# Kernel optimization log

Hardware: AMD Instinct MI355X
Metric: run time of the kernel (lower is better)

## Reference

```python
import jax
import jax.numpy as jnp
from jax import lax
import numpy as np

B, H, W, C = 8, 128, 128, 64
KH, KW = 3, 3
K = KH * KW
OUT = 64
PAD = 1  # 'same' padding for 3x3, stride 1, dilation 1


def setup_inputs() -> dict:
    key = jax.random.key(0)
    k1, k2, k3, k4 = jax.random.split(key, 4)
    scale = 0.05  # keep learned offsets in a sane pixel range
    x = jax.random.normal(k1, (B, H, W, C), dtype=jnp.float32)
    offset_kernel = jax.random.normal(k2, (KH, KW, C, 2 * K), dtype=jnp.float32) * scale
    mask_kernel = jax.random.normal(k3, (KH, KW, C, K), dtype=jnp.float32) * scale
    filt = jax.random.normal(k4, (OUT, C, KH, KW), dtype=jnp.float32) * scale
    return {"x": x, "offset_kernel": offset_kernel, "mask_kernel": mask_kernel, "filt": filt}


def _conv_same(x, kernel):
    # x: [B,H,W,C], kernel: [kh,kw,Cin,Cout] -> [B,H,W,Cout]
    return lax.conv_general_dilated(
        x, kernel, window_strides=(1, 1), padding='SAME',
        dimension_numbers=('NHWC', 'HWIO', 'NHWC'))


def _bilinear_gather(img, py, px):
    # img: [B,C,H,W]; py,px: [B,K,H,W] float sampling coords (zero outside image)
    b, c, h, w = img.shape
    imf = img.reshape(b, c, h * w)
    y0 = jnp.floor(py)
    x0 = jnp.floor(px)
    ly = py - y0
    lx = px - x0

    def corner(yi, xi, wgt):
        valid = (yi >= 0) & (yi <= h - 1) & (xi >= 0) & (xi <= w - 1)
        yc = jnp.clip(yi, 0, h - 1).astype(jnp.int32)
        xc = jnp.clip(xi, 0, w - 1).astype(jnp.int32)
        idx = yc * w + xc  # [B,K,H,W]
        v = jax.vmap(lambda im, ix: jnp.take(im, ix, axis=1))(imf, idx)  # [B,C,K,H,W]
        return v * (wgt * valid.astype(img.dtype))[:, None]

    return (corner(y0, x0, (1 - ly) * (1 - lx))
            + corner(y0, x0 + 1, (1 - ly) * lx)
            + corner(y0 + 1, x0, ly * (1 - lx))
            + corner(y0 + 1, x0 + 1, ly * lx))


def reference(x, offset_kernel, mask_kernel, filt):
    # offset conv and mask conv (mask goes through sigmoid), both channels_last
    offset = _conv_same(x, offset_kernel)                 # [B,H,W,2K]
    mask = jax.nn.sigmoid(_conv_same(x, mask_kernel))     # [B,H,W,K]

    xc = jnp.transpose(x, (0, 3, 1, 2))                   # [B,C,H,W]
    off = jnp.transpose(offset, (0, 3, 1, 2)).reshape(B, K, 2, H, W)
    dy, dx = off[:, :, 0], off[:, :, 1]                   # [B,K,H,W]
    m = jnp.transpose(mask, (0, 3, 1, 2))                 # [B,K,H,W]

    # base sampling grid: p = out_loc + kernel_offset - pad + learned offset
    hh = jnp.arange(H, dtype=jnp.float32)
    ww = jnp.arange(W, dtype=jnp.float32)
    ky = jnp.repeat(jnp.arange(KH, dtype=jnp.float32), KW)  # [K]
    kx = jnp.tile(jnp.arange(KW, dtype=jnp.float32), KH)    # [K]
    py = hh[None, None, :, None] + (ky - PAD)[None, :, None, None] + dy  # [B,K,H,W]
    px = ww[None, None, None, :] + (kx - PAD)[None, :, None, None] + dx

    cols = _bilinear_gather(xc, py, px)                   # [B,C,K,H,W]
    cols = cols * m[:, None]                              # modulated (offset_groups=1)

    fk = filt.reshape(OUT, C, K)
    out = jnp.einsum('bcknm,ock->bonm', cols, fk)         # [B,OUT,H,W]
    return jnp.transpose(out, (0, 2, 3, 1))               # NHWC, bias disabled
```

## Files before the change

### kernel.cpp

```cpp
#include <hip/hip_runtime.h>
#include <math.h>

#define BB 8
#define HH 128
#define WW 128
#define CC 64
#define KK 9
#define OUTC 64
#define TW 16
#define KTOT 576
#define NELEM (BB*HH*WW*CC)
#define XSW 3456

typedef __attribute__((ext_vector_type(8))) short short8v;
typedef __attribute__((ext_vector_type(4))) float float4v;

static __device__ __forceinline__ unsigned short f2bf(float f) {
    unsigned int u = __float_as_uint(f);
    return (unsigned short)((u + 0x7FFFu + ((u >> 16) & 1u)) >> 16);
}
static __device__ __forceinline__ float bf2f(unsigned short h) {
    return __uint_as_float(((unsigned int)h) << 16);
}
static __device__ __forceinline__ float bf2f_lo(unsigned int w) {
    return __uint_as_float(w << 16);
}
static __device__ __forceinline__ float bf2f_hi(unsigned int w) {
    return __uint_as_float(w & 0xFFFF0000u);
}

static __device__ __forceinline__ int frag_addr(int p, int kappa) {
    int chunk = kappa >> 3;
    return ((chunk >> 2) << 9) + ((chunk & 3) << 7) + ((p ^ (chunk & 7)) << 3) + (kappa & 7);
}

__global__ __launch_bounds__(256) void prep_all(
    const float* __restrict__ x, const float* __restrict__ offk,
    const float* __restrict__ mk, const float* __restrict__ filt,
    unsigned short* __restrict__ fbf,
    unsigned short* __restrict__ wcf,
    unsigned short* __restrict__ xh,
    unsigned short* __restrict__ xl,
    int do_x)
{
    int bid = blockIdx.x, tid = threadIdx.x;
    if (bid < 144) {
        int j = bid * 256 + tid;
        {
            int w = j / 9216, rem = j - w * 9216;
            int ks = rem >> 9, ln = (rem >> 3) & 63, sj = rem & 7;
            int pl = ln & 15, lg = ln >> 4;
            int o = w * 16 + pl, kap = ks * 32 + lg * 8 + sj;
            int k = kap >> 6, c = kap & 63;
            fbf[j] = f2bf(filt[(o * CC + c) * KK + k]);
        }
        if (j < 18432) {
            int nh = j / 9216, rem = j - nh * 9216;
            int ks = rem >> 9, ln = (rem >> 3) & 63, sj = rem & 7;
            int pl = ln & 15, lg = ln >> 4;
            int o = nh * 16 + pl, kap = ks * 32 + lg * 8 + sj;
            int k = kap >> 6, c = kap & 63;
            float v = 0.f;
            if (o < 18)      v = offk[(k * CC + c) * 18 + o];
            else if (o < 27) v = mk[(k * CC + c) * 9 + (o - 18)];
            wcf[j] = f2bf(v);
        }
        return;
    }
    if (!do_x) return;
    int i = (bid - 144) * 256 + tid;
    const float* src = x + (size_t)i * 8;
    float4 a = *(const float4*)(src);
    float4 c = *(const float4*)(src + 4);
    float v[8] = {a.x, a.y, a.z, a.w, c.x, c.y, c.z, c.w};
    unsigned hq[4], lq[4];
#pragma unroll
    for (int j = 0; j < 4; ++j) {
        unsigned short h0 = f2bf(v[2 * j]),     h1 = f2bf(v[2 * j + 1]);
        unsigned short l0 = f2bf(v[2 * j] - bf2f(h0));
        unsigned short l1 = f2bf(v[2 * j + 1] - bf2f(h1));
        hq[j] = (unsigned)h0 | ((unsigned)h1 << 16);
        lq[j] = (unsigned)l0 | ((unsigned)l1 << 16);
    }
    *(uint4*)(xh + (size_t)i * 8) = make_uint4(hq[0], hq[1], hq[2], hq[3]);
    *(uint4*)(xl + (size_t)i * 8) = make_uint4(lq[0], lq[1], lq[2], lq[3]);
}

template<int HASB>
__global__ __launch_bounds__(256, 7) void deform_conv_fused(
    const float* __restrict__ x,
    const unsigned short* __restrict__ xh,
    const unsigned short* __restrict__ xl,
    const unsigned short* __restrict__ fbf,
    const unsigned short* __restrict__ wcf,
    float* __restrict__ out)
{
    __shared__ __align__(16) unsigned short ims[TW * KTOT];
    __shared__ __align__(16) union UU {
        float ps2[4][TW][18];
        struct { int4 c[144]; float4 w[144]; } gs;
    } u;

    const int tid  = threadIdx.x;
    const int lane = tid & 63;
    const int wave = tid >> 6;
    const int pl = lane & 15;
    const int lg = lane >> 4;
    const int off_e = lg * 128 + ((pl ^ lg) << 3);
    const int off_o = lg * 128 + ((pl ^ (lg + 4)) << 3);

    const int swz = (blockIdx.x & 7) * 1024 + (blockIdx.x >> 3);
    const int bw = swz & 7;
    const int h  = (swz >> 3) & 127;
    const int b  = swz >> 10;
    const int w0 = bw * TW;

    for (int e = tid; e < 864; e += 256) {
        int pln  = e / 432;
        int rem  = e - pln * 432;
        int r    = rem / 144;
        int rem2 = rem - r * 144;
        int px   = rem2 >> 3;
        int c8   = rem2 & 7;
        int y = h + r - 1, xg = w0 + px - 1;
        int lidx = (r * 18 + px) * 64 + ((c8 * 8) ^ ((px & 7) << 3)) + pln * XSW;
        uint4 val = make_uint4(0u, 0u, 0u, 0u);
        if ((unsigned)y < (unsigned)HH && (unsigned)xg < (unsigned)WW) {
            int goff = ((b * HH + y) * WW + xg) * CC + c8 * 8;
            if (HASB) {
                val = *(const uint4*)((pln ? xl : xh) + goff);
            } else {
                float4 v0 = *(const float4*)(x + goff);
                float4 v1 = *(const float4*)(x + goff + 4);
                float vv[8] = {v0.x, v0.y, v0.z, v0.w, v1.x, v1.y, v1.z, v1.w};
                unsigned short q[8];
#pragma unroll
                for (int j = 0; j < 8; ++j) {
                    unsigned short h0 = f2bf(vv[j]);
                    q[j] = pln ? f2bf(vv[j] - bf2f(h0)) : h0;
                }
                val = make_uint4((unsigned)q[0] | ((unsigned)q[1] << 16),
                                 (unsigned)q[2] | ((unsigned)q[3] << 16),
                                 (unsigned)q[4] | ((unsigned)q[5] << 16),
                                 (unsigned)q[6] | ((unsigned)q[7] << 16));
            }
        }
        *(uint4*)(ims + lidx) = val;
    }
    __syncthreads();

    const int nh = wave & 1, kh = wave >> 1;
    float4v acch = {0.f, 0.f, 0.f, 0.f}, accl = {0.f, 0.f, 0.f, 0.f};
    __builtin_amdgcn_s_setprio(1);
#pragma unroll
    for (int ks9 = 0; ks9 < 9; ++ks9) {
        const int ksg = kh * 9 + ks9;
        const int tap = ksg >> 1;
        const int cb  = (ksg & 1) * 32 + lg * 8;
        const int ky = tap / 3, kx = tap - ky * 3;
        const int px = pl + kx;
        const int base = (ky * 18 + px) * 64 + (cb ^ ((px & 7) << 3));
        short8v ahf = *(const short8v*)(ims + base);
        short8v alf = *(const short8v*)(ims + XSW + base);
        short8v bv  = *(const short8v*)(wcf + ((nh * 18 + ksg) << 9) + (lane << 3));
        acch = __builtin_amdgcn_mfma_f32_16x16x32_bf16(ahf, bv, acch, 0, 0, 0);
        accl = __builtin_amdgcn_mfma_f32_16x16x32_bf16(alf, bv, accl, 0, 0, 0);
    }
    __builtin_amdgcn_s_setprio(0);
#pragma unroll
    for (int r = 0; r < 4; ++r)
        u.ps2[wave][lg * 4 + r][pl] = acch[r] + accl[r];

    const unsigned short* Bpf = fbf + ((wave * 18) << 9) + (lane << 3);
    short8v bp0 = *(const short8v*)(Bpf);
    short8v bp1 = *(const short8v*)(Bpf + 512);
    __syncthreads();

    const int sp = tid / 9, sk = tid - (tid / 9) * 9;
    float s_dy = 0.f, s_dx = 0.f, s_ml = 0.f;
    if (tid < 144) {
        auto rd = [&](int o) {
            int nhh = o >> 4, col = o & 15;
            return u.ps2[nhh][sp][col] + u.ps2[2 + nhh][sp][col];
        };
        s_dy = rd(2 * sk); s_dx = rd(2 * sk + 1); s_ml = rd(18 + sk);
    }
    __syncthreads();

    if (tid < 144) {
        float m  = 1.f / (1.f + __expf(-s_ml));
        float py = (float)(h + (sk / 3) - 1) + s_dy;
        float px = (float)(w0 + sp + (sk % 3) - 1) + s_dx;
        float y0 = floorf(py), x0 = floorf(px);
        float ly = py - y0, lx = px - x0;
        bool vy0 = (y0 >= 0.f)  && (y0 <= 127.f);
        bool vy1 = (y0 >= -1.f) && (y0 <= 126.f);
        bool vx0 = (x0 >= 0.f)  && (x0 <= 127.f);
        bool vx1 = (x0 >= -1.f) && (x0 <= 126.f);
        float wy0 = 1.f - ly, wx0 = 1.f - lx;
        int iy0 = (int)fminf(fmaxf(y0, 0.f), 127.f);
        int iy1 = (int)fminf(fmaxf(y0 + 1.f, 0.f), 127.f);
        int ix0 = (int)fminf(fmaxf(x0, 0.f), 127.f);
        int ix1 = (int)fminf(fmaxf(x0 + 1.f, 0.f), 127.f);
        int base = b * (HH * WW * CC);
        u.gs.c[tid] = make_int4(base + (iy0 * WW + ix0) * CC,
                                base + (iy0 * WW + ix1) * CC,
                                base + (iy1 * WW + ix0) * CC,
                                base + (iy1 * WW + ix1) * CC);
        u.gs.w[tid] = make_float4((vy0 && vx0) ? wy0 * wx0 * m : 0.f,
                                  (vy0 && vx1) ? wy0 * lx  * m : 0.f,
                                  (vy1 && vx0) ? ly  * wx0 * m : 0.f,
                                  (vy1 && vx1) ? ly  * lx  * m : 0.f);
    }
    __syncthreads();

    if (HASB) {
        for (int t = tid; t < 1152; t += 256) {
            int pair = t >> 3, c8 = t & 7;
            int p = pair / 9, k = pair - (pair / 9) * 9;
            int4   cc = u.gs.c[pair];
            float4 wv = u.gs.w[pair];
            int co = c8 * 8;
            uint4 u00 = *(const uint4*)(xh + cc.x + co);
            uint4 u01 = *(const uint4*)(xh + cc.y + co);
            uint4 u10 = *(const uint4*)(xh + cc.z + co);
            uint4 u11 = *(const uint4*)(xh + cc.w + co);
            const unsigned* a00 = (const unsigned*)&u00;
            const unsigned* a01 = (const unsigned*)&u01;
            const unsigned* a10 = (const unsigned*)&u10;
            const unsigned* a11 = (const unsigned*)&u11;
            unsigned qq[4];
#pragma unroll
            for (int jj = 0; jj < 4; ++jj) {
                float rl = wv.x * bf2f_lo(a00[jj]) + wv.y * bf2f_lo(a01[jj])
                         + wv.z * bf2f_lo(a10[jj]) + wv.w * bf2f_lo(a11[jj]);
                float rh = wv.x * bf2f_hi(a00[jj]) + wv.y * bf2f_hi(a01[jj])
                         + wv.z * bf2f_hi(a10[jj]) + wv.w * bf2f_hi(a11[jj]);
                qq[jj] = (unsigned)f2bf(rl) | ((unsigned)f2bf(rh) << 16);
            }
            *(uint4*)(ims + frag_addr(p, k * 64 + co)) = make_uint4(qq[0], qq[1], qq[2], qq[3]);
        }
    } else {
        for (int t = tid; t < 1152; t += 256) {
            int pair = t >> 3, c8 = t & 7;
            int p = pair / 9, k = pair - (pair / 9) * 9;
            int4   cc = u.gs.c[pair];
            float4 wv = u.gs.w[pair];
            int co = c8 * 8;
            float r[8];
#pragma unroll
            for (int half = 0; half < 2; ++half) {
                float4 v00 = *(const float4*)(x + cc.x + co + half * 4);
                float4 v01 = *(const float4*)(x + cc.y + co + half * 4);
                float4 v10 = *(const float4*)(x + cc.z + co + half * 4);
                float4 v11 = *(const float4*)(x + cc.w + co + half * 4);
                r[half * 4 + 0] = wv.x * v00.x + wv.y * v01.x + wv.z * v10.x + wv.w * v11.x;
                r[half * 4 + 1] = wv.x * v00.y + wv.y * v01.y + wv.z * v10.y + wv.w * v11.y;
                r[half * 4 + 2] = wv.x * v00.z + wv.y * v01.z + wv.z * v10.z + wv.w * v11.z;
                r[half * 4 + 3] = wv.x * v00.w + wv.y * v01.w + wv.z * v10.w + wv.w * v11.w;
            }
            unsigned qq[4];
#pragma unroll
            for (int jj = 0; jj < 4; ++jj)
                qq[jj] = (unsigned)f2bf(r[2 * jj]) | ((unsigned)f2bf(r[2 * jj + 1]) << 16);
            *(uint4*)(ims + frag_addr(p, k * 64 + co)) = make_uint4(qq[0], qq[1], qq[2], qq[3]);
        }
    }
    __syncthreads();

    {
        float4v accA = {0.f, 0.f, 0.f, 0.f}, accB = {0.f, 0.f, 0.f, 0.f};
        __builtin_amdgcn_s_setprio(1);
#pragma unroll
        for (int ks = 0; ks < 18; ++ks) {
            short8v a  = *(const short8v*)(ims + ks * 512 + ((ks & 1) ? off_o : off_e));
            short8v bv = (ks == 0) ? bp0 : (ks == 1) ? bp1
                       : *(const short8v*)(Bpf + (ks << 9));
            if (ks & 1) accB = __builtin_amdgcn_mfma_f32_16x16x32_bf16(a, bv, accB, 0, 0, 0);
            else        accA = __builtin_amdgcn_mfma_f32_16x16x32_bf16(a, bv, accA, 0, 0, 0);
        }
        __builtin_amdgcn_s_setprio(0);
        const int o = wave * 16 + pl;
        const size_t rowbase = (size_t)(b * HH + h) * WW + w0;
#pragma unroll
        for (int r = 0; r < 4; ++r) {
            int p = lg * 4 + r;
            out[(rowbase + p) * OUTC + o] = accA[r] + accB[r];
        }
    }
}

extern "C" void kernel_launch(void* const* d_in, const int* in_sizes, int n_in,
                              void* d_out, int out_size, void* d_ws, size_t ws_size,
                              hipStream_t stream) {
    const float* x    = (const float*)d_in[0];
    const float* offk = (const float*)d_in[1];
    const float* mk   = (const float*)d_in[2];
    const float* filt = (const float*)d_in[3];
    float* out = (float*)d_out;
    unsigned short* fbf = (unsigned short*)d_ws;
    unsigned short* wcf = fbf + OUTC * KTOT;
    unsigned short* xh  = wcf + 32 * KTOT;
    unsigned short* xl  = xh + NELEM;
    size_t need = (size_t)(OUTC + 32) * KTOT * 2 + (size_t)NELEM * 4;
    int do_x = (ws_size >= need) ? 1 : 0;
    prep_all<<<144 + (do_x ? 4096 : 0), 256, 0, stream>>>(x, offk, mk, filt, fbf, wcf, xh, xl, do_x);
    if (do_x)
        deform_conv_fused<1><<<BB * HH * (WW / TW), 256, 0, stream>>>(x, xh, xl, fbf, wcf, out);
    else
        deform_conv_fused<0><<<BB * HH * (WW / TW), 256, 0, stream>>>(x, xh, xl, fbf, wcf, out);
}
```

Before: 80.09 us.

## Switch from split-bf16 to single fp16 storage and fp16 MFMA

Replaces the hi/lo bf16 split of x with one fp16 copy, so the offset/mask conv needs one MFMA stream instead of two, and prep writes half the data. The main MFMA now runs in f16 with the same instruction shape. Bilinear sampling weights are stored as packed half2 and the interpolation uses __hfma2 packed-half arithmetic. This cuts prep-time memory traffic, LDS staging and gather bandwidth. The cost is precision: fp16 has less range than bf16, and accumulating the interpolation in half may change the results.

```diff
diff --git a/kernel.cpp b/kernel.cpp
--- a/kernel.cpp
+++ b/kernel.cpp
@@ -1,4 +1,5 @@
 #include <hip/hip_runtime.h>
+#include <hip/hip_fp16.h>
 #include <math.h>
 
 #define BB 8
@@ -12,21 +13,18 @@
 #define NELEM (BB*HH*WW*CC)
 #define XSW 3456
 
-typedef __attribute__((ext_vector_type(8))) short short8v;
+typedef __attribute__((ext_vector_type(8))) _Float16 half8v;
 typedef __attribute__((ext_vector_type(4))) float float4v;
 
-static __device__ __forceinline__ unsigned short f2bf(float f) {
-    unsigned int u = __float_as_uint(f);
-    return (unsigned short)((u + 0x7FFFu + ((u >> 16) & 1u)) >> 16);
-}
-static __device__ __forceinline__ float bf2f(unsigned short h) {
-    return __uint_as_float(((unsigned int)h) << 16);
-}
-static __device__ __forceinline__ float bf2f_lo(unsigned int w) {
-    return __uint_as_float(w << 16);
-}
-static __device__ __forceinline__ float bf2f_hi(unsigned int w) {
-    return __uint_as_float(w & 0xFFFF0000u);
+static __device__ __forceinline__ unsigned short f2h(float f) {
+    return __half_as_ushort(__float2half(f));
+}
+static __device__ __forceinline__ unsigned h2bits(float f) {
+    __half2 h = __float2half2_rn(f);
+    unsigned r; __builtin_memcpy(&r, &h, 4); return r;
+}
+static __device__ __forceinline__ __half2 bits2h(unsigned w) {
+    __half2 h; __builtin_memcpy(&h, &w, 4); return h;
 }
 
 static __device__ __forceinline__ int frag_addr(int p, int kappa) {
@@ -39,8 +37,7 @@
     const float* __restrict__ mk, const float* __restrict__ filt,
     unsigned short* __restrict__ fbf,
     unsigned short* __restrict__ wcf,
-    unsigned short* __restrict__ xh,
-    unsigned short* __restrict__ xl,
+    unsigned short* __restrict__ xf,
     int do_x)
 {
     int bid = blockIdx.x, tid = threadIdx.x;
@@ -52,7 +49,7 @@
             int pl = ln & 15, lg = ln >> 4;
             int o = w * 16 + pl, kap = ks * 32 + lg * 8 + sj;
             int k = kap >> 6, c = kap & 63;
-            fbf[j] = f2bf(filt[(o * CC + c) * KK + k]);
+            fbf[j] = f2h(filt[(o * CC + c) * KK + k]);
         }
         if (j < 18432) {
             int nh = j / 9216, rem = j - nh * 9216;
@@ -63,7 +60,7 @@
             float v = 0.f;
             if (o < 18)      v = offk[(k * CC + c) * 18 + o];
             else if (o < 27) v = mk[(k * CC + c) * 9 + (o - 18)];
-            wcf[j] = f2bf(v);
+            wcf[j] = f2h(v);
         }
         return;
     }
@@ -73,24 +70,17 @@
     float4 a = *(const float4*)(src);
     float4 c = *(const float4*)(src + 4);
     float v[8] = {a.x, a.y, a.z, a.w, c.x, c.y, c.z, c.w};
-    unsigned hq[4], lq[4];
-#pragma unroll
-    for (int j = 0; j < 4; ++j) {
-        unsigned short h0 = f2bf(v[2 * j]),     h1 = f2bf(v[2 * j + 1]);
-        unsigned short l0 = f2bf(v[2 * j] - bf2f(h0));
-        unsigned short l1 = f2bf(v[2 * j + 1] - bf2f(h1));
-        hq[j] = (unsigned)h0 | ((unsigned)h1 << 16);
-        lq[j] = (unsigned)l0 | ((unsigned)l1 << 16);
-    }
-    *(uint4*)(xh + (size_t)i * 8) = make_uint4(hq[0], hq[1], hq[2], hq[3]);
-    *(uint4*)(xl + (size_t)i * 8) = make_uint4(lq[0], lq[1], lq[2], lq[3]);
+    unsigned q[4];
+#pragma unroll
+    for (int j = 0; j < 4; ++j)
+        q[j] = (unsigned)f2h(v[2 * j]) | ((unsigned)f2h(v[2 * j + 1]) << 16);
+    *(uint4*)(xf + (size_t)i * 8) = make_uint4(q[0], q[1], q[2], q[3]);
 }
 
 template<int HASB>
 __global__ __launch_bounds__(256, 7) void deform_conv_fused(
     const float* __restrict__ x,
-    const unsigned short* __restrict__ xh,
-    const unsigned short* __restrict__ xl,
+    const unsigned short* __restrict__ xf,
     const unsigned short* __restrict__ fbf,
     const unsigned short* __restrict__ wcf,
     float* __restrict__ out)
@@ -98,7 +88,7 @@
     __shared__ __align__(16) unsigned short ims[TW * KTOT];
     __shared__ __align__(16) union UU {
         float ps2[4][TW][18];
-        struct { int4 c[144]; float4 w[144]; } gs;
+        struct { int4 c[144]; uint4 w[144]; } gs;
     } u;
 
     const int tid  = threadIdx.x;
@@ -115,34 +105,30 @@
     const int b  = swz >> 10;
     const int w0 = bw * TW;
 
-    for (int e = tid; e < 864; e += 256) {
-        int pln  = e / 432;
-        int rem  = e - pln * 432;
-        int r    = rem / 144;
-        int rem2 = rem - r * 144;
+#pragma unroll
+    for (int it = 0; it < 2; ++it) {
+        int e = tid + it * 256;
+        if (it == 1 && e >= 432) break;
+        int r    = (e >= 288) ? 2 : (e >= 144) ? 1 : 0;
+        int rem2 = e - r * 144;
         int px   = rem2 >> 3;
         int c8   = rem2 & 7;
         int y = h + r - 1, xg = w0 + px - 1;
-        int lidx = (r * 18 + px) * 64 + ((c8 * 8) ^ ((px & 7) << 3)) + pln * XSW;
+        int lidx = (r * 18 + px) * 64 + ((c8 * 8) ^ ((px & 7) << 3));
         uint4 val = make_uint4(0u, 0u, 0u, 0u);
         if ((unsigned)y < (unsigned)HH && (unsigned)xg < (unsigned)WW) {
             int goff = ((b * HH + y) * WW + xg) * CC + c8 * 8;
             if (HASB) {
-                val = *(const uint4*)((pln ? xl : xh) + goff);
+                val = *(const uint4*)(xf + goff);
             } else {
                 float4 v0 = *(const float4*)(x + goff);
                 float4 v1 = *(const float4*)(x + goff + 4);
                 float vv[8] = {v0.x, v0.y, v0.z, v0.w, v1.x, v1.y, v1.z, v1.w};
-                unsigned short q[8];
-#pragma unroll
-                for (int j = 0; j < 8; ++j) {
-                    unsigned short h0 = f2bf(vv[j]);
-                    q[j] = pln ? f2bf(vv[j] - bf2f(h0)) : h0;
-                }
-                val = make_uint4((unsigned)q[0] | ((unsigned)q[1] << 16),
-                                 (unsigned)q[2] | ((unsigned)q[3] << 16),
-                                 (unsigned)q[4] | ((unsigned)q[5] << 16),
-                                 (unsigned)q[6] | ((unsigned)q[7] << 16));
+                unsigned q[4];
+#pragma unroll
+                for (int j = 0; j < 4; ++j)
+                    q[j] = (unsigned)f2h(vv[2 * j]) | ((unsigned)f2h(vv[2 * j + 1]) << 16);
+                val = make_uint4(q[0], q[1], q[2], q[3]);
             }
         }
         *(uint4*)(ims + lidx) = val;
@@ -150,7 +136,7 @@
     __syncthreads();
 
     const int nh = wave & 1, kh = wave >> 1;
-    float4v acch = {0.f, 0.f, 0.f, 0.f}, accl = {0.f, 0.f, 0.f, 0.f};
+    float4v acc = {0.f, 0.f, 0.f, 0.f};
     __builtin_amdgcn_s_setprio(1);
 #pragma unroll
     for (int ks9 = 0; ks9 < 9; ++ks9) {
@@ -160,20 +146,18 @@
         const int ky = tap / 3, kx = tap - ky * 3;
         const int px = pl + kx;
         const int base = (ky * 18 + px) * 64 + (cb ^ ((px & 7) << 3));
-        short8v ahf = *(const short8v*)(ims + base);
-        short8v alf = *(const short8v*)(ims + XSW + base);
-        short8v bv  = *(const short8v*)(wcf + ((nh * 18 + ksg) << 9) + (lane << 3));
-        acch = __builtin_amdgcn_mfma_f32_16x16x32_bf16(ahf, bv, acch, 0, 0, 0);
-        accl = __builtin_amdgcn_mfma_f32_16x16x32_bf16(alf, bv, accl, 0, 0, 0);
+        half8v af = *(const half8v*)(ims + base);
+        half8v bv = *(const half8v*)(wcf + ((nh * 18 + ksg) << 9) + (lane << 3));
+        acc = __builtin_amdgcn_mfma_f32_16x16x32_f16(af, bv, acc, 0, 0, 0);
     }
     __builtin_amdgcn_s_setprio(0);
 #pragma unroll
     for (int r = 0; r < 4; ++r)
-        u.ps2[wave][lg * 4 + r][pl] = acch[r] + accl[r];
+        u.ps2[wave][lg * 4 + r][pl] = acc[r];
 
     const unsigned short* Bpf = fbf + ((wave * 18) << 9) + (lane << 3);
-    short8v bp0 = *(const short8v*)(Bpf);
-    short8v bp1 = *(const short8v*)(Bpf + 512);
+    half8v bp0 = *(const half8v*)(Bpf);
+    half8v bp1 = *(const half8v*)(Bpf + 512);
     __syncthreads();
 
     const int sp = tid / 9, sk = tid - (tid / 9) * 9;
@@ -207,10 +191,10 @@
                                 base + (iy0 * WW + ix1) * CC,
                                 base + (iy1 * WW + ix0) * CC,
                                 base + (iy1 * WW + ix1) * CC);
-        u.gs.w[tid] = make_float4((vy0 && vx0) ? wy0 * wx0 * m : 0.f,
-                                  (vy0 && vx1) ? wy0 * lx  * m : 0.f,
-                                  (vy1 && vx0) ? ly  * wx0 * m : 0.f,
-                                  (vy1 && vx1) ? ly  * lx  * m : 0.f);
+        u.gs.w[tid] = make_uint4(h2bits((vy0 && vx0) ? wy0 * wx0 * m : 0.f),
+                                 h2bits((vy0 && vx1) ? wy0 * lx  * m : 0.f),
+                                 h2bits((vy1 && vx0) ? ly  * wx0 * m : 0.f),
+                                 h2bits((vy1 && vx1) ? ly  * lx  * m : 0.f));
     }
     __syncthreads();
 
@@ -218,13 +202,15 @@
         for (int t = tid; t < 1152; t += 256) {
             int pair = t >> 3, c8 = t & 7;
             int p = pair / 9, k = pair - (pair / 9) * 9;
-            int4   cc = u.gs.c[pair];
-            float4 wv = u.gs.w[pair];
+            int4  cc = u.gs.c[pair];
+            uint4 wq = u.gs.w[pair];
+            __half2 w0 = bits2h(wq.x), w1 = bits2h(wq.y);
+            __half2 w2 = bits2h(wq.z), w3 = bits2h(wq.w);
             int co = c8 * 8;
-            uint4 u00 = *(const uint4*)(xh + cc.x + co);
-            uint4 u01 = *(const uint4*)(xh + cc.y + co);
-            uint4 u10 = *(const uint4*)(xh + cc.z + co);
-            uint4 u11 = *(const uint4*)(xh + cc.w + co);
+            uint4 u00 = *(const uint4*)(xf + cc.x + co);
+            uint4 u01 = *(const uint4*)(xf + cc.y + co);
+            uint4 u10 = *(const uint4*)(xf + cc.z + co);
+            uint4 u11 = *(const uint4*)(xf + cc.w + co);
             const unsigned* a00 = (const unsigned*)&u00;
             const unsigned* a01 = (const unsigned*)&u01;
             const unsigned* a10 = (const unsigned*)&u10;
@@ -232,11 +218,11 @@
             unsigned qq[4];
 #pragma unroll
             for (int jj = 0; jj < 4; ++jj) {
-                float rl = wv.x * bf2f_lo(a00[jj]) + wv.y * bf2f_lo(a01[jj])
-                         + wv.z * bf2f_lo(a10[jj]) + wv.w * bf2f_lo(a11[jj]);
-                float rh = wv.x * bf2f_hi(a00[jj]) + wv.y * bf2f_hi(a01[jj])
-                         + wv.z * bf2f_hi(a10[jj]) + wv.w * bf2f_hi(a11[jj]);
-                qq[jj] = (unsigned)f2bf(rl) | ((unsigned)f2bf(rh) << 16);
+                __half2 acc2 = __hmul2(bits2h(a00[jj]), w0);
+                acc2 = __hfma2(bits2h(a01[jj]), w1, acc2);
+                acc2 = __hfma2(bits2h(a10[jj]), w2, acc2);
+                acc2 = __hfma2(bits2h(a11[jj]), w3, acc2);
+                __builtin_memcpy(&qq[jj], &acc2, 4);
             }
             *(uint4*)(ims + frag_addr(p, k * 64 + co)) = make_uint4(qq[0], qq[1], qq[2], qq[3]);
         }
@@ -244,8 +230,12 @@
         for (int t = tid; t < 1152; t += 256) {
             int pair = t >> 3, c8 = t & 7;
             int p = pair / 9, k = pair - (pair / 9) * 9;
-            int4   cc = u.gs.c[pair];
-            float4 wv = u.gs.w[pair];
+            int4  cc = u.gs.c[pair];
+            uint4 wq = u.gs.w[pair];
+            float wx = __half2float(bits2h(wq.x).x);
+            float wy = __half2float(bits2h(wq.y).x);
+            float wz = __half2float(bits2h(wq.z).x);
+            float ww = __half2float(bits2h(wq.w).x);
             int co = c8 * 8;
             float r[8];
 #pragma unroll
@@ -254,15 +244,15 @@
                 float4 v01 = *(const float4*)(x + cc.y + co + half * 4);
                 float4 v10 = *(const float4*)(x + cc.z + co + half * 4);
                 float4 v11 = *(const float4*)(x + cc.w + co + half * 4);
-                r[half * 4 + 0] = wv.x * v00.x + wv.y * v01.x + wv.z * v10.x + wv.w * v11.x;
-                r[half * 4 + 1] = wv.x * v00.y + wv.y * v01.y + wv.z * v10.y + wv.w * v11.y;
-                r[half * 4 + 2] = wv.x * v00.z + wv.y * v01.z + wv.z * v10.z + wv.w * v11.z;
-                r[half * 4 + 3] = wv.x * v00.w + wv.y * v01.w + wv.z * v10.w + wv.w * v11.w;
+                r[half * 4 + 0] = wx * v00.x + wy * v01.x + wz * v10.x + ww * v11.x;
+                r[half * 4 + 1] = wx * v00.y + wy * v01.y + wz * v10.y + ww * v11.y;
+                r[half * 4 + 2] = wx * v00.z + wy * v01.z + wz * v10.z + ww * v11.z;
+                r[half * 4 + 3] = wx * v00.w + wy * v01.w + wz * v10.w + ww * v11.w;
             }
             unsigned qq[4];
 #pragma unroll
             for (int jj = 0; jj < 4; ++jj)
-                qq[jj] = (unsigned)f2bf(r[2 * jj]) | ((unsigned)f2bf(r[2 * jj + 1]) << 16);
+                qq[jj] = (unsigned)f2h(r[2 * jj]) | ((unsigned)f2h(r[2 * jj + 1]) << 16);
             *(uint4*)(ims + frag_addr(p, k * 64 + co)) = make_uint4(qq[0], qq[1], qq[2], qq[3]);
         }
     }
@@ -273,11 +263,11 @@
         __builtin_amdgcn_s_setprio(1);
 #pragma unroll
         for (int ks = 0; ks < 18; ++ks) {
-            short8v a  = *(const short8v*)(ims + ks * 512 + ((ks & 1) ? off_o : off_e));
-            short8v bv = (ks == 0) ? bp0 : (ks == 1) ? bp1
-                       : *(const short8v*)(Bpf + (ks << 9));
-            if (ks & 1) accB = __builtin_amdgcn_mfma_f32_16x16x32_bf16(a, bv, accB, 0, 0, 0);
-            else        accA = __builtin_amdgcn_mfma_f32_16x16x32_bf16(a, bv, accA, 0, 0, 0);
+            half8v a  = *(const half8v*)(ims + ks * 512 + ((ks & 1) ? off_o : off_e));
+            half8v bv = (ks == 0) ? bp0 : (ks == 1) ? bp1
+                      : *(const half8v*)(Bpf + (ks << 9));
+            if (ks & 1) accB = __builtin_amdgcn_mfma_f32_16x16x32_f16(a, bv, accB, 0, 0, 0);
+            else        accA = __builtin_amdgcn_mfma_f32_16x16x32_f16(a, bv, accA, 0, 0, 0);
         }
         __builtin_amdgcn_s_setprio(0);
         const int o = wave * 16 + pl;
@@ -300,13 +290,12 @@
     float* out = (float*)d_out;
     unsigned short* fbf = (unsigned short*)d_ws;
     unsigned short* wcf = fbf + OUTC * KTOT;
-    unsigned short* xh  = wcf + 32 * KTOT;
-    unsigned short* xl  = xh + NELEM;
-    size_t need = (size_t)(OUTC + 32) * KTOT * 2 + (size_t)NELEM * 4;
+    unsigned short* xf  = wcf + 32 * KTOT;
+    size_t need = (size_t)(OUTC + 32) * KTOT * 2 + (size_t)NELEM * 2;
     int do_x = (ws_size >= need) ? 1 : 0;
-    prep_all<<<144 + (do_x ? 4096 : 0), 256, 0, stream>>>(x, offk, mk, filt, fbf, wcf, xh, xl, do_x);
+    prep_all<<<144 + (do_x ? 4096 : 0), 256, 0, stream>>>(x, offk, mk, filt, fbf, wcf, xf, do_x);
     if (do_x)
-        deform_conv_fused<1><<<BB * HH * (WW / TW), 256, 0, stream>>>(x, xh, xl, fbf, wcf, out);
+        deform_conv_fused<1><<<BB * HH * (WW / TW), 256, 0, stream>>>(x, xf, fbf, wcf, out);
     else
-        deform_conv_fused<0><<<BB * HH * (WW / TW), 256, 0, stream>>>(x, xh, xl, fbf, wcf, out);
-}
+        deform_conv_fused<0><<<BB * HH * (WW / TW), 256, 0, stream>>>(x, xf, fbf, wcf, out);
+}
```

Result: faster. 65.72 us (median of 2 runs) (-17.9%).
